# Performance work log

Measured on AMD Instinct MI355X. Metric: run time of the kernel, lower is better.

## Reference

```python
import jax, jax.numpy as jnp
import numpy as np
import math

D_MODEL = 1024
N_HEADS = 16
D_K = D_MODEL // N_HEADS
FFN = 4096
B, S = 4, 1024
EPS = 1e-5


def setup_inputs() -> dict:
    key = jax.random.key(0)
    ks = jax.random.split(key, 24)
    sd = 0.02
    def w(k, shape):
        return jax.random.normal(k, shape, dtype=jnp.float32) * sd
    inp = {
        'x': jax.random.normal(ks[0], (B, S, D_MODEL), dtype=jnp.float32),
        'enc': jax.random.normal(ks[1], (B, S, D_MODEL), dtype=jnp.float32),
        'mask': jnp.tril(jnp.ones((S, S), dtype=jnp.int32)),  # causal look-ahead mask
        # stacked per-head projections [H, d_model, d_k], biases [H, d_k]
        'Wq_self': w(ks[2], (N_HEADS, D_MODEL, D_K)), 'bq_self': w(ks[3], (N_HEADS, D_K)),
        'Wk_self': w(ks[4], (N_HEADS, D_MODEL, D_K)), 'bk_self': w(ks[5], (N_HEADS, D_K)),
        'Wv_self': w(ks[6], (N_HEADS, D_MODEL, D_K)), 'bv_self': w(ks[7], (N_HEADS, D_K)),
        'Wq_x': w(ks[8], (N_HEADS, D_MODEL, D_K)), 'bq_x': w(ks[9], (N_HEADS, D_K)),
        'Wk_x': w(ks[10], (N_HEADS, D_MODEL, D_K)), 'bk_x': w(ks[11], (N_HEADS, D_K)),
        'Wv_x': w(ks[12], (N_HEADS, D_MODEL, D_K)), 'bv_x': w(ks[13], (N_HEADS, D_K)),
        # W_O is SHARED between self- and cross-attention (as in the torch code)
        'Wo': w(ks[14], (D_MODEL, D_MODEL)), 'bo': w(ks[15], (D_MODEL,)),
        'W1': w(ks[16], (D_MODEL, FFN)), 'b1': w(ks[17], (FFN,)),
        'W2': w(ks[18], (FFN, D_MODEL)), 'b2': w(ks[19], (D_MODEL,)),
        'g1': jnp.ones((D_MODEL,), jnp.float32), 'be1': jnp.zeros((D_MODEL,), jnp.float32),
        'g2': jnp.ones((D_MODEL,), jnp.float32), 'be2': jnp.zeros((D_MODEL,), jnp.float32),
        'g3': jnp.ones((D_MODEL,), jnp.float32), 'be3': jnp.zeros((D_MODEL,), jnp.float32),
    }
    return inp


def _layernorm(x, g, b):
    mu = jnp.mean(x, axis=-1, keepdims=True)
    d = x - mu
    var = jnp.mean(d * d, axis=-1, keepdims=True)
    return d * jax.lax.rsqrt(var + EPS) * g + b


def _mha(xq, xkv, Wq, bq, Wk, bk, Wv, bv, mask):
    # batched equivalent of the per-head Python loop
    q = jnp.einsum('bsd,hdk->bhsk', xq, Wq) + bq[None, :, None, :]
    k = jnp.einsum('btd,hdk->bhtk', xkv, Wk) + bk[None, :, None, :]
    v = jnp.einsum('btd,hdk->bhtk', xkv, Wv) + bv[None, :, None, :]
    scores = jnp.einsum('bhsk,bhtk->bhst', q, k) / math.sqrt(D_K)
    if mask is not None:
        scores = jnp.where(mask[None, None] == 0, -jnp.inf, scores)
    attn = jax.nn.softmax(scores, axis=-1)
    z = jnp.einsum('bhst,bhtk->bhsk', attn, v)
    # concat heads along last dim (head i occupies slice i, matching torch.cat)
    b_, h_, s_, k_ = z.shape
    return jnp.transpose(z, (0, 2, 1, 3)).reshape(b_, s_, h_ * k_)


def reference(x, enc, mask, Wq_self, bq_self, Wk_self, bk_self, Wv_self, bv_self,
              Wq_x, bq_x, Wk_x, bk_x, Wv_x, bv_x, Wo, bo, W1, b1, W2, b2,
              g1, be1, g2, be2, g3, be3):
    sa = _mha(x, x, Wq_self, bq_self, Wk_self, bk_self, Wv_self, bv_self, mask)
    x1 = _layernorm(x + sa @ Wo + bo, g1, be1)
    ca = _mha(x1, enc, Wq_x, bq_x, Wk_x, bk_x, Wv_x, bv_x, None)
    x2 = _layernorm(x1 + ca @ Wo + bo, g2, be2)
    ffn = jax.nn.relu(x2 @ W1 + b1) @ W2 + b2
    return _layernorm(x2 + ffn, g3, be3)
```

## Files before the change

### kernel.cpp

```cpp
#include <hip/hip_runtime.h>
#include <cstdint>

typedef __bf16 bf16_t;
typedef bf16_t bf16x8 __attribute__((ext_vector_type(8)));
typedef bf16_t bf16x4 __attribute__((ext_vector_type(4)));
typedef float  f32x4  __attribute__((ext_vector_type(4)));

#define DEVI static __device__ __forceinline__

DEVI void async_ld16(const bf16_t* g, bf16_t* l) {
  __builtin_amdgcn_global_load_lds((const __attribute__((address_space(1))) void*)g,
                                   (__attribute__((address_space(3))) void*)l, 16, 0, 0);
}

struct PrepArgs {
  const float *WqS, *WkS, *WvS, *WqX, *WkX, *WvX, *Wo, *W1, *W2, *x, *enc;
  const float *bqS, *bkS, *bvS, *bkX, *bvX;
  bf16_t *WqkvST, *WqXT, *WkvXT, *WoT, *W1T, *W2T, *xb, *encb;
  float *bqkv, *bkvx;
};

__global__ __launch_bounds__(256)
void k_prep(PrepArgs a)
{
  __shared__ float tile[32][36];
  const int blk = blockIdx.x, tid = threadIdx.x;

  const float* src = nullptr;
  bf16_t* dst = nullptr;
  int srcLd = 0, dstLd = 0, m0 = 0, n0 = 0;
  bool do_tr = false;

  if (blk < 6144) {
    int j = blk >> 10, q = blk & 1023;
    src = j == 0 ? a.WqS : j == 1 ? a.WkS : j == 2 ? a.WvS : j == 3 ? a.WqX : j == 4 ? a.WkX : a.WvX;
    dst = j == 0 ? a.WqkvST : j == 1 ? a.WqkvST + 1048576 : j == 2 ? a.WqkvST + 2097152
        : j == 3 ? a.WqXT : j == 4 ? a.WkvXT : a.WkvXT + 1048576;
    int batch = q >> 6, rem = q & 63;
    src += (long)batch * 65536; dst += (long)batch * 65536;
    srcLd = 64; dstLd = 1024;
    n0 = (rem & 1) * 32; m0 = (rem >> 1) * 32;
    do_tr = true;
  } else if (blk < 7168) {
    int q = blk - 6144;
    src = a.Wo; dst = a.WoT; srcLd = 1024; dstLd = 1024;
    m0 = (q >> 5) * 32; n0 = (q & 31) * 32; do_tr = true;
  } else if (blk < 11264) {
    int q = blk - 7168;
    src = a.W1; dst = a.W1T; srcLd = 4096; dstLd = 1024;
    m0 = (q >> 7) * 32; n0 = (q & 127) * 32; do_tr = true;
  } else if (blk < 15360) {
    int q = blk - 11264;
    src = a.W2; dst = a.W2T; srcLd = 1024; dstLd = 4096;
    m0 = (q >> 5) * 32; n0 = (q & 31) * 32; do_tr = true;
  } else if (blk < 16384) {
    long base = (long)(blk - 15360) * 4096 + tid * 4;
#pragma unroll
    for (int u = 0; u < 4; u++) {
      float4 v = *(const float4*)(a.x + base + u * 1024);
      bf16x4 o; o[0] = (bf16_t)v.x; o[1] = (bf16_t)v.y; o[2] = (bf16_t)v.z; o[3] = (bf16_t)v.w;
      *(bf16x4*)(a.xb + base + u * 1024) = o;
    }
    return;
  } else if (blk < 17408) {
    long base = (long)(blk - 16384) * 4096 + tid * 4;
#pragma unroll
    for (int u = 0; u < 4; u++) {
      float4 v = *(const float4*)(a.enc + base + u * 1024);
      bf16x4 o; o[0] = (bf16_t)v.x; o[1] = (bf16_t)v.y; o[2] = (bf16_t)v.z; o[3] = (bf16_t)v.w;
      *(bf16x4*)(a.encb + base + u * 1024) = o;
    }
    return;
  } else {
    int gi = (blk - 17408) * 1024 + tid * 4;
#pragma unroll
    for (int j = 0; j < 4; j++) {
      int i = gi + j;
      if (i < 1024)      a.bqkv[i] = a.bqS[i];
      else if (i < 2048) a.bqkv[i] = a.bkS[i - 1024];
      else if (i < 3072) a.bqkv[i] = a.bvS[i - 2048];
      else if (i < 4096) a.bkvx[i - 3072] = a.bkX[i - 3072];
      else if (i < 5120) a.bkvx[i - 3072] = a.bvX[i - 4096];
    }
    return;
  }

  if (do_tr) {
    {
      int r = tid >> 3, c4 = (tid & 7) * 4;
      *(float4*)&tile[r][c4] = *(const float4*)(src + (long)(m0 + r) * srcLd + n0 + c4);
    }
    __syncthreads();
    {
      int nr = tid >> 3, mq = (tid & 7) * 4;
      bf16x4 o;
      o[0] = (bf16_t)tile[mq + 0][nr];
      o[1] = (bf16_t)tile[mq + 1][nr];
      o[2] = (bf16_t)tile[mq + 2][nr];
      o[3] = (bf16_t)tile[mq + 3][nr];
      *(bf16x4*)(dst + (long)(n0 + nr) * dstLd + m0 + mq) = o;
    }
  }
}

template<int OUT_MODE, int RELU, int VOFF>
__global__ __launch_bounds__(256, 2)
void k_gemm(const bf16_t* __restrict__ A, int lda,
            const bf16_t* __restrict__ Bt, int ldb,
            const float* __restrict__ bias,
            bf16_t* __restrict__ C, int ldc,
            bf16_t* __restrict__ Vt,
            bf16_t* __restrict__ p0, bf16_t* __restrict__ p1,
            bf16_t* __restrict__ p2, bf16_t* __restrict__ p3,
            int Ktot, int nx)
{
  __shared__ bf16_t As[2][128 * 32];
  __shared__ bf16_t Bs[2][128 * 32];
  const int tid  = threadIdx.x;
  const int wave = tid >> 6, lane = tid & 63;
  const int quad = lane >> 4, m16 = lane & 15;

  int lin = blockIdx.x;
  int perx = gridDim.x >> 3;
  int t = (lin & 7) * perx + (lin >> 3);
  const int bcol = (t % nx) * 128, brow = (t / nx) * 128;
  const int wr = (wave >> 1) * 64, wc = (wave & 1) * 64;

  const int Kper = Ktot / gridDim.z;
  const int k0 = blockIdx.z * Kper;

  f32x4 acc[4][4];
#pragma unroll
  for (int i = 0; i < 4; i++)
#pragma unroll
    for (int j = 0; j < 4; j++) acc[i][j] = (f32x4){0.f, 0.f, 0.f, 0.f};

  auto stage = [&](int kt, int buf) {
#pragma unroll
    for (int i = 0; i < 2; i++) {
      int rg = wave * 2 + i;
      async_ld16(A  + (long)(brow + rg * 16 + m16) * lda + kt + quad * 8, As[buf] + rg * 512);
      async_ld16(Bt + (long)(bcol + rg * 16 + m16) * ldb + kt + quad * 8, Bs[buf] + rg * 512);
    }
  };

  stage(k0, 0);
  __syncthreads();

  const int nIter = Kper >> 5;
  for (int it = 0; it < nIter; it++) {
    const int cur = it & 1;
    if (it + 1 < nIter) stage(k0 + (it + 1) * 32, cur ^ 1);

    bf16x8 af[4], bfr[4];
#pragma unroll
    for (int tt = 0; tt < 4; tt++) {
      af[tt]  = *(const bf16x8*)(As[cur] + ((wr + tt * 16) >> 4) * 512 + quad * 128 + m16 * 8);
      bfr[tt] = *(const bf16x8*)(Bs[cur] + ((wc + tt * 16) >> 4) * 512 + quad * 128 + m16 * 8);
    }
#pragma unroll
    for (int i = 0; i < 4; i++)
#pragma unroll
      for (int j = 0; j < 4; j++)
        acc[i][j] = __builtin_amdgcn_mfma_f32_16x16x32_bf16(af[i], bfr[j], acc[i][j], 0, 0, 0);

    __syncthreads();
  }

  if (OUT_MODE == 1) {
    bf16_t* P = blockIdx.z == 0 ? p0 : blockIdx.z == 1 ? p1 : blockIdx.z == 2 ? p2 : p3;
#pragma unroll
    for (int i = 0; i < 4; i++)
#pragma unroll
      for (int j = 0; j < 4; j++) {
        int col = bcol + wc + j * 16 + m16;
#pragma unroll
        for (int r = 0; r < 4; r++) {
          int row = brow + wr + i * 16 + quad * 4 + r;
          P[(long)row * ldc + col] = (bf16_t)acc[i][j][r];
        }
      }
  } else {
#pragma unroll
    for (int i = 0; i < 4; i++)
#pragma unroll
      for (int j = 0; j < 4; j++) {
        int col = bcol + wc + j * 16 + m16;
        float bv = bias[col];
        if (VOFF && col >= VOFF) {
          int hh = (col - VOFF) >> 6, dd = col & 63;
          int row0 = brow + wr + i * 16 + quad * 4;
          int bb = row0 >> 10, seq = row0 & 1023;
          bf16x4 pk;
#pragma unroll
          for (int r = 0; r < 4; r++) pk[r] = (bf16_t)(acc[i][j][r] + bv);
          *(bf16x4*)(Vt + (long)(bb * 16 + hh) * 65536 + dd * 1024 + seq) = pk;
        } else {
#pragma unroll
          for (int r = 0; r < 4; r++) {
            int row = brow + wr + i * 16 + quad * 4 + r;
            float v = acc[i][j][r] + bv;
            if (RELU) v = v > 0.f ? v : 0.f;
            C[(long)row * ldc + col] = (bf16_t)v;
          }
        }
      }
  }
}

template<int OUT_MODE, int RELU, int VOFF>
__global__ __launch_bounds__(512, 2)
void k_gemm256(const bf16_t* __restrict__ A, int lda,
               const bf16_t* __restrict__ Bt, int ldb,
               const float* __restrict__ bias,
               bf16_t* __restrict__ C, int ldc,
               bf16_t* __restrict__ Vt,
               bf16_t* __restrict__ p0, bf16_t* __restrict__ p1,
               bf16_t* __restrict__ p2, bf16_t* __restrict__ p3,
               int Ktot, int nx)
{
  __shared__ bf16_t As[2][256 * 64];
  __shared__ bf16_t Bs[2][256 * 64];
  const int tid  = threadIdx.x;
  const int wave = tid >> 6, lane = tid & 63;
  const int quad = lane >> 4, m16 = lane & 15;

  int lin = blockIdx.x;
  int perx = gridDim.x >> 3;
  int t = (lin & 7) * perx + (lin >> 3);
  const int bcol = (t % nx) * 256, brow = (t / nx) * 256;
  const int wr = (wave >> 2) * 128, wc = (wave & 3) * 64;

  const int Kper = Ktot / gridDim.z;
  const int k0 = blockIdx.z * Kper;

  f32x4 acc[8][4];
#pragma unroll
  for (int i = 0; i < 8; i++)
#pragma unroll
    for (int j = 0; j < 4; j++) acc[i][j] = (f32x4){0.f, 0.f, 0.f, 0.f};

  auto stage = [&](int kt, int buf) {
#pragma unroll
    for (int i = 0; i < 2; i++) {
      int rg = wave * 2 + i;
#pragma unroll
      for (int ks = 0; ks < 2; ks++) {
        async_ld16(A  + (long)(brow + rg * 16 + m16) * lda + kt + ks * 32 + quad * 8,
                   As[buf] + (rg * 2 + ks) * 512);
        async_ld16(Bt + (long)(bcol + rg * 16 + m16) * ldb + kt + ks * 32 + quad * 8,
                   Bs[buf] + (rg * 2 + ks) * 512);
      }
    }
  };

  stage(k0, 0);
  __syncthreads();

  const int nIter = Kper >> 6;
  for (int it = 0; it < nIter; it++) {
    const int cur = it & 1;
    if (it + 1 < nIter) stage(k0 + (it + 1) * 64, cur ^ 1);

    const bf16_t* Ac = As[cur];
    const bf16_t* Bc = Bs[cur];
#pragma unroll
    for (int ks = 0; ks < 2; ks++) {
      bf16x8 af[8], bfr[4];
#pragma unroll
      for (int tt = 0; tt < 8; tt++)
        af[tt] = *(const bf16x8*)(Ac + (((wr + tt * 16) >> 4) * 2 + ks) * 512 + quad * 128 + m16 * 8);
#pragma unroll
      for (int j = 0; j < 4; j++)
        bfr[j] = *(const bf16x8*)(Bc + (((wc + j * 16) >> 4) * 2 + ks) * 512 + quad * 128 + m16 * 8);
      __builtin_amdgcn_s_setprio(1);
#pragma unroll
      for (int i = 0; i < 8; i++)
#pragma unroll
        for (int j = 0; j < 4; j++)
          acc[i][j] = __builtin_amdgcn_mfma_f32_16x16x32_bf16(af[i], bfr[j], acc[i][j], 0, 0, 0);
      __builtin_amdgcn_s_setprio(0);
    }

    __syncthreads();
  }

  if (OUT_MODE == 1) {
    bf16_t* P = blockIdx.z == 0 ? p0 : blockIdx.z == 1 ? p1 : blockIdx.z == 2 ? p2 : p3;
#pragma unroll
    for (int i = 0; i < 8; i++)
#pragma unroll
      for (int j = 0; j < 4; j++) {
        int col = bcol + wc + j * 16 + m16;
#pragma unroll
        for (int r = 0; r < 4; r++) {
          int row = brow + wr + i * 16 + quad * 4 + r;
          P[(long)row * ldc + col] = (bf16_t)acc[i][j][r];
        }
      }
  } else {
#pragma unroll
    for (int i = 0; i < 8; i++)
#pragma unroll
      for (int j = 0; j < 4; j++) {
        int col = bcol + wc + j * 16 + m16;
        float bv = bias[col];
        if (VOFF && col >= VOFF) {
          int hh = (col - VOFF) >> 6, dd = col & 63;
          int row0 = brow + wr + i * 16 + quad * 4;
          int bb = row0 >> 10, seq = row0 & 1023;
          bf16x4 pk;
#pragma unroll
          for (int r = 0; r < 4; r++) pk[r] = (bf16_t)(acc[i][j][r] + bv);
          *(bf16x4*)(Vt + (long)(bb * 16 + hh) * 65536 + dd * 1024 + seq) = pk;
        } else {
#pragma unroll
          for (int r = 0; r < 4; r++) {
            int row = brow + wr + i * 16 + quad * 4 + r;
            float v = acc[i][j][r] + bv;
            if (RELU) v = v > 0.f ? v : 0.f;
            C[(long)row * ldc + col] = (bf16_t)v;
          }
        }
      }
  }
}

template<int LN, int RESID, int OUTF, int OUTB, int NPART>
__global__ __launch_bounds__(256)
void k_reduceN(const bf16_t* __restrict__ p0, const bf16_t* __restrict__ p1,
               const bf16_t* __restrict__ p2, const bf16_t* __restrict__ p3,
               const float* __restrict__ bias, const float* __restrict__ resid,
               const float* __restrict__ gamma, const float* __restrict__ beta,
               float* __restrict__ outf, bf16_t* __restrict__ outb)
{
  constexpr int D = 1024;
  __shared__ float red[8];
  int row = blockIdx.x, tid = threadIdx.x;
  long off = (long)row * D + tid * 4;
  bf16x4 a0 = *(const bf16x4*)(p0 + off);
  bf16x4 a1 = *(const bf16x4*)(p1 + off);
  float4 bb4 = *(const float4*)(bias + tid * 4);
  float4 v;
  v.x = (float)a0[0] + (float)a1[0] + bb4.x;
  v.y = (float)a0[1] + (float)a1[1] + bb4.y;
  v.z = (float)a0[2] + (float)a1[2] + bb4.z;
  v.w = (float)a0[3] + (float)a1[3] + bb4.w;
  if (NPART == 4) {
    bf16x4 a2 = *(const bf16x4*)(p2 + off);
    bf16x4 a3 = *(const bf16x4*)(p3 + off);
    v.x += (float)a2[0] + (float)a3[0];
    v.y += (float)a2[1] + (float)a3[1];
    v.z += (float)a2[2] + (float)a3[2];
    v.w += (float)a2[3] + (float)a3[3];
  }
  if (RESID) {
    float4 q = *(const float4*)(resid + off);
    v.x += q.x; v.y += q.y; v.z += q.z; v.w += q.w;
  }
  float4 y = v;
  if (LN) {
    float s  = v.x + v.y + v.z + v.w;
    float sq = v.x * v.x + v.y * v.y + v.z * v.z + v.w * v.w;
#pragma unroll
    for (int o = 1; o < 64; o <<= 1) {
      s  += __shfl_xor(s, o, 64);
      sq += __shfl_xor(sq, o, 64);
    }
    int wave = tid >> 6, lane = tid & 63;
    if (lane == 0) { red[wave * 2] = s; red[wave * 2 + 1] = sq; }
    __syncthreads();
    float ts = red[0] + red[2] + red[4] + red[6];
    float tq = red[1] + red[3] + red[5] + red[7];
    float mu = ts * (1.f / D);
    float var = tq * (1.f / D) - mu * mu;
    float rstd = rsqrtf(var + 1e-5f);
    float4 g  = *(const float4*)(gamma + tid * 4);
    float4 be = *(const float4*)(beta + tid * 4);
    y.x = (v.x - mu) * rstd * g.x + be.x;
    y.y = (v.y - mu) * rstd * g.y + be.y;
    y.z = (v.z - mu) * rstd * g.z + be.z;
    y.w = (v.w - mu) * rstd * g.w + be.w;
  }
  if (OUTF) *(float4*)(outf + off) = y;
  if (OUTB) {
    bf16x4 o;
    o[0] = (bf16_t)y.x; o[1] = (bf16_t)y.y; o[2] = (bf16_t)y.z; o[3] = (bf16_t)y.w;
    *(bf16x4*)(outb + off) = o;
  }
}

template<int CAUSAL>
__global__ __launch_bounds__(256, 2)
void k_attn(const bf16_t* __restrict__ Q, int ldq,
            const bf16_t* __restrict__ Kp, int ldk,
            const bf16_t* __restrict__ Vt,
            bf16_t* __restrict__ O)
{
  constexpr int S = 1024;
  __shared__ bf16_t Kls[2][4096];
  __shared__ bf16_t Vls[2][4096];
  __shared__ bf16_t Pls[4][32 * 72];

  const int tid = threadIdx.x;
  const int wave = tid >> 6, lane = tid & 63;
  const int quad = lane >> 4, m16 = lane & 15;
  const int bh = blockIdx.y, b = bh >> 4, h = bh & 15;
  const int qt = (CAUSAL && (bh & 32)) ? ((int)gridDim.x - 1 - (int)blockIdx.x)
                                       : (int)blockIdx.x;
  const int qbase = qt * 128 + wave * 32;

  bf16x8 qf[2][2];
#pragma unroll
  for (int rh = 0; rh < 2; rh++) {
    const bf16_t* qp = Q + (long)(b * S + qbase + rh * 16 + m16) * ldq + h * 64 + quad * 8;
    qf[rh][0] = *(const bf16x8*)qp;
    qf[rh][1] = *(const bf16x8*)(qp + 32);
  }

  f32x4 o_acc[2][4];
#pragma unroll
  for (int rh = 0; rh < 2; rh++)
#pragma unroll
    for (int t = 0; t < 4; t++) o_acc[rh][t] = (f32x4){0.f, 0.f, 0.f, 0.f};
  float rsum[2][4];
#pragma unroll
  for (int rh = 0; rh < 2; rh++)
#pragma unroll
    for (int r = 0; r < 4; r++) rsum[rh][r] = 0.f;

  auto stage = [&](int c, int buf) {
#pragma unroll
    for (int i = 0; i < 2; i++) {
      int t2 = wave * 2 + i;
      int rg = t2 & 3, ph = t2 >> 2;
      async_ld16(Kp + (long)(b * S + c * 64 + rg * 16 + m16) * ldk + h * 64 + ph * 32 + quad * 8,
                 Kls[buf] + t2 * 512);
      async_ld16(Vt + (long)bh * 65536 + (rg * 16 + m16) * 1024 + c * 64 + ph * 32 + quad * 8,
                 Vls[buf] + t2 * 512);
    }
  };

  const int nch = CAUSAL ? (2 * qt + 2) : 16;
  stage(0, 0);

  for (int c = 0; c < nch; c++) {
    __syncthreads();
    const int cur = c & 1;
    if (c + 1 < nch) stage(c + 1, cur ^ 1);

    f32x4 s[2][4];
#pragma unroll
    for (int t = 0; t < 4; t++) {
      bf16x8 k0 = *(const bf16x8*)(Kls[cur] + (0 * 4 + t) * 512 + quad * 128 + m16 * 8);
      bf16x8 k1 = *(const bf16x8*)(Kls[cur] + (1 * 4 + t) * 512 + quad * 128 + m16 * 8);
      __builtin_amdgcn_s_setprio(1);
#pragma unroll
      for (int rh = 0; rh < 2; rh++) {
        f32x4 z = (f32x4){0.f, 0.f, 0.f, 0.f};
        z = __builtin_amdgcn_mfma_f32_16x16x32_bf16(qf[rh][0], k0, z, 0, 0, 0);
        z = __builtin_amdgcn_mfma_f32_16x16x32_bf16(qf[rh][1], k1, z, 0, 0, 0);
        s[rh][t] = z;
      }
      __builtin_amdgcn_s_setprio(0);
    }

    bf16_t* pw = Pls[wave];
#pragma unroll
    for (int rh = 0; rh < 2; rh++)
#pragma unroll
      for (int r = 0; r < 4; r++) {
        int qg = qbase + rh * 16 + quad * 4 + r;
#pragma unroll
        for (int t = 0; t < 4; t++) {
          float v = s[rh][t][r] * 0.125f;
          float p;
          if (CAUSAL) {
            int kvg = c * 64 + t * 16 + m16;
            p = (kvg <= qg) ? __expf(v) : 0.f;
          } else {
            p = __expf(v);
          }
          rsum[rh][r] += p;
          pw[(rh * 16 + quad * 4 + r) * 72 + t * 16 + m16] = (bf16_t)p;
        }
      }

    bf16x8 pf[2][2];
#pragma unroll
    for (int rh = 0; rh < 2; rh++)
#pragma unroll
      for (int kvh = 0; kvh < 2; kvh++)
        pf[rh][kvh] = *(const bf16x8*)(pw + (rh * 16 + m16) * 72 + kvh * 32 + quad * 8);
#pragma unroll
    for (int t = 0; t < 4; t++) {
      bf16x8 v0 = *(const bf16x8*)(Vls[cur] + (0 * 4 + t) * 512 + quad * 128 + m16 * 8);
      bf16x8 v1 = *(const bf16x8*)(Vls[cur] + (1 * 4 + t) * 512 + quad * 128 + m16 * 8);
      __builtin_amdgcn_s_setprio(1);
#pragma unroll
      for (int rh = 0; rh < 2; rh++) {
        o_acc[rh][t] = __builtin_amdgcn_mfma_f32_16x16x32_bf16(pf[rh][0], v0, o_acc[rh][t], 0, 0, 0);
        o_acc[rh][t] = __builtin_amdgcn_mfma_f32_16x16x32_bf16(pf[rh][1], v1, o_acc[rh][t], 0, 0, 0);
      }
      __builtin_amdgcn_s_setprio(0);
    }
  }

#pragma unroll
  for (int rh = 0; rh < 2; rh++)
#pragma unroll
    for (int r = 0; r < 4; r++) {
      float v = rsum[rh][r];
      v += __shfl_xor(v, 1, 64);
      v += __shfl_xor(v, 2, 64);
      v += __shfl_xor(v, 4, 64);
      v += __shfl_xor(v, 8, 64);
      rsum[rh][r] = 1.f / v;
    }
#pragma unroll
  for (int rh = 0; rh < 2; rh++)
#pragma unroll
    for (int t = 0; t < 4; t++)
#pragma unroll
      for (int r = 0; r < 4; r++) {
        int row = b * S + qbase + rh * 16 + quad * 4 + r;
        int col = h * 64 + t * 16 + m16;
        O[(long)row * 1024 + col] = (bf16_t)(o_acc[rh][t][r] * rsum[rh][r]);
      }
}

extern "C" void kernel_launch(void* const* d_in, const int* in_sizes, int n_in,
                              void* d_out, int out_size, void* d_ws, size_t ws_size,
                              hipStream_t stream)
{
  const float* x   = (const float*)d_in[0];
  const float* enc = (const float*)d_in[1];
  const float* WqS = (const float*)d_in[3];
  const float* bqS = (const float*)d_in[4];
  const float* WkS = (const float*)d_in[5];
  const float* bkS = (const float*)d_in[6];
  const float* WvS = (const float*)d_in[7];
  const float* bvS = (const float*)d_in[8];
  const float* WqX = (const float*)d_in[9];
  const float* bqX = (const float*)d_in[10];
  const float* WkX = (const float*)d_in[11];
  const float* bkX = (const float*)d_in[12];
  const float* WvX = (const float*)d_in[13];
  const float* bvX = (const float*)d_in[14];
  const float* Wo  = (const float*)d_in[15];
  const float* bo  = (const float*)d_in[16];
  const float* W1  = (const float*)d_in[17];
  const float* b1  = (const float*)d_in[18];
  const float* W2  = (const float*)d_in[19];
  const float* b2  = (const float*)d_in[20];
  const float* g1  = (const float*)d_in[21];
  const float* be1 = (const float*)d_in[22];
  const float* g2  = (const float*)d_in[23];
  const float* be2 = (const float*)d_in[24];
  const float* g3  = (const float*)d_in[25];
  const float* be3 = (const float*)d_in[26];

  char* ws = (char*)d_ws;
  const long MBy = 1048576;
  bf16_t* WqkvST = (bf16_t*)(ws + 0 * MBy);
  bf16_t* WqXT   = (bf16_t*)(ws + 6 * MBy);
  bf16_t* WkvXT  = (bf16_t*)(ws + 8 * MBy);
  bf16_t* WoT    = (bf16_t*)(ws + 12 * MBy);
  bf16_t* W1T    = (bf16_t*)(ws + 14 * MBy);
  bf16_t* W2T    = (bf16_t*)(ws + 22 * MBy);
  float*  bqkvS  = (float*)(ws + 30 * MBy);
  float*  bkvX   = (float*)(ws + 30 * MBy + 16384);
  bf16_t* xb     = (bf16_t*)(ws + 31 * MBy);
  bf16_t* Qx     = xb;
  bf16_t* encb   = (bf16_t*)(ws + 39 * MBy);
  float*  x1f    = (float*)(ws + 47 * MBy);
  bf16_t* x1b    = (bf16_t*)(ws + 63 * MBy);
  bf16_t* Z      = (bf16_t*)(ws + 71 * MBy);
  bf16_t* QK     = (bf16_t*)(ws + 79 * MBy);
  bf16_t* Kenc   = (bf16_t*)(ws + 79 * MBy);
  bf16_t* Vt     = (bf16_t*)(ws + 95 * MBy);
  bf16_t* pa0 = (bf16_t*)(ws + 95 * MBy);
  bf16_t* pa1 = (bf16_t*)(ws + 103 * MBy);
  bf16_t* Hbuf = (bf16_t*)(ws + 95 * MBy);
  bf16_t* pf0 = (bf16_t*)(ws + 0 * MBy);
  bf16_t* pf1 = (bf16_t*)(ws + 8 * MBy);
  bf16_t* pf2 = (bf16_t*)(ws + 31 * MBy);
  bf16_t* pf3 = (bf16_t*)(ws + 39 * MBy);

  dim3 tb(256), tb512(512);

  PrepArgs pa;
  pa.WqS = WqS; pa.WkS = WkS; pa.WvS = WvS; pa.WqX = WqX; pa.WkX = WkX; pa.WvX = WvX;
  pa.Wo = Wo; pa.W1 = W1; pa.W2 = W2; pa.x = x; pa.enc = enc;
  pa.bqS = bqS; pa.bkS = bkS; pa.bvS = bvS; pa.bkX = bkX; pa.bvX = bvX;
  pa.WqkvST = WqkvST; pa.WqXT = WqXT; pa.WkvXT = WkvXT; pa.WoT = WoT;
  pa.W1T = W1T; pa.W2T = W2T; pa.xb = xb; pa.encb = encb;
  pa.bqkv = bqkvS; pa.bkvx = bkvX;
  k_prep<<<dim3(17413), tb, 0, stream>>>(pa);

  k_gemm<0, 0, 2048><<<dim3(768, 1, 1), tb, 0, stream>>>(
      xb, 1024, WqkvST, 1024, bqkvS, QK, 2048, Vt,
      nullptr, nullptr, nullptr, nullptr, 1024, 24);
  k_attn<1><<<dim3(8, 64), tb, 0, stream>>>(QK, 2048, QK + 1024, 2048, Vt, Z);
  k_gemm<1, 0, 0><<<dim3(256, 1, 2), tb, 0, stream>>>(
      Z, 1024, WoT, 1024, nullptr, nullptr, 1024, nullptr,
      pa0, pa1, nullptr, nullptr, 1024, 8);
  k_reduceN<1, 1, 1, 1, 2><<<dim3(4096), tb, 0, stream>>>(
      pa0, pa1, nullptr, nullptr, bo, x, g1, be1, x1f, x1b);

  k_gemm<1, 0, 0><<<dim3(256, 1, 2), tb, 0, stream>>>(
      x1b, 1024, WqXT, 1024, nullptr, nullptr, 1024, nullptr,
      pa0, pa1, nullptr, nullptr, 1024, 8);
  k_reduceN<0, 0, 0, 1, 2><<<dim3(4096), tb, 0, stream>>>(
      pa0, pa1, nullptr, nullptr, bqX, nullptr, nullptr, nullptr, nullptr, Qx);
  k_gemm<0, 0, 1024><<<dim3(512, 1, 1), tb, 0, stream>>>(
      encb, 1024, WkvXT, 1024, bkvX, Kenc, 1024, Vt,
      nullptr, nullptr, nullptr, nullptr, 1024, 16);
  k_attn<0><<<dim3(8, 64), tb, 0, stream>>>(Qx, 1024, Kenc, 1024, Vt, Z);
  k_gemm<1, 0, 0><<<dim3(256, 1, 2), tb, 0, stream>>>(
      Z, 1024, WoT, 1024, nullptr, nullptr, 1024, nullptr,
      pa0, pa1, nullptr, nullptr, 1024, 8);
  k_reduceN<1, 1, 1, 1, 2><<<dim3(4096), tb, 0, stream>>>(
      pa0, pa1, nullptr, nullptr, bo, x1f, g2, be2, x1f, x1b);

  k_gemm256<0, 1, 0><<<dim3(256, 1, 1), tb512, 0, stream>>>(
      x1b, 1024, W1T, 1024, b1, Hbuf, 4096, nullptr,
      nullptr, nullptr, nullptr, nullptr, 1024, 16);
  k_gemm256<1, 0, 0><<<dim3(64, 1, 4), tb512, 0, stream>>>(
      Hbuf, 4096, W2T, 4096, nullptr, nullptr, 1024, nullptr,
      pf0, pf1, pf2, pf3, 4096, 4);
  k_reduceN<1, 1, 1, 0, 4><<<dim3(4096), tb, 0, stream>>>(
      pf0, pf1, pf2, pf3, b2, x1f, g3, be3, (float*)d_out, nullptr);
}
```

Measured before the change: 546.1 us.

## Merge cross-attention Q and KV projections into one dual GEMM launch

Adds a dual-role GEMM kernel whose blocks split by index into the Qx projection (from x1) and the encoder K/V projection, so both run in one launch without the split-K partials and reduction pass for Qx. The self-attention QKV projection also moves to the larger 256-tile GEMM kernel with fewer blocks. This removes two launches and a round trip through partial buffers, and fills the GPU with the union of both grids. In exchange, the new kernel uses smaller 128x128 tiles with K-step 32 and no split-K, and the bigger tile for QKV leaves fewer blocks to spread across CUs.

After: 538.4 us. No clear change (-1.4%).

```diff
diff --git a/kernel.cpp b/kernel.cpp
--- a/kernel.cpp
+++ b/kernel.cpp
@@ -206,6 +206,97 @@
         }
       }
   }
+}
+
+__global__ __launch_bounds__(256, 2)
+void k_gemm_dual(const bf16_t* __restrict__ Aa, const bf16_t* __restrict__ Bta,
+                 const float* __restrict__ biasa, bf16_t* __restrict__ Ca,
+                 int nxa, int nblkA,
+                 const bf16_t* __restrict__ Ab, const bf16_t* __restrict__ Btb,
+                 const float* __restrict__ biasb, bf16_t* __restrict__ Cb,
+                 int nxb,
+                 bf16_t* __restrict__ Vt)
+{
+  __shared__ bf16_t As[2][128 * 32];
+  __shared__ bf16_t Bs[2][128 * 32];
+  const int tid  = threadIdx.x;
+  const int wave = tid >> 6, lane = tid & 63;
+  const int quad = lane >> 4, m16 = lane & 15;
+
+  const bool roleB = (int)blockIdx.x >= nblkA;
+  const bf16_t* A    = roleB ? Ab    : Aa;
+  const bf16_t* Bt   = roleB ? Btb   : Bta;
+  const float*  bias = roleB ? biasb : biasa;
+  bf16_t*       C    = roleB ? Cb    : Ca;
+  const int nx   = roleB ? nxb : nxa;
+  const int lin  = roleB ? ((int)blockIdx.x - nblkA) : (int)blockIdx.x;
+  const int nblk = roleB ? ((int)gridDim.x - nblkA) : nblkA;
+  const int perx = nblk >> 3;
+  const int t = (lin & 7) * perx + (lin >> 3);
+  const int bcol = (t % nx) * 128, brow = (t / nx) * 128;
+  const int wr = (wave >> 1) * 64, wc = (wave & 1) * 64;
+  const int lda = 1024, ldb = 1024, ldc = 1024;
+
+  f32x4 acc[4][4];
+#pragma unroll
+  for (int i = 0; i < 4; i++)
+#pragma unroll
+    for (int j = 0; j < 4; j++) acc[i][j] = (f32x4){0.f, 0.f, 0.f, 0.f};
+
+  auto stage = [&](int kt, int buf) {
+#pragma unroll
+    for (int i = 0; i < 2; i++) {
+      int rg = wave * 2 + i;
+      async_ld16(A  + (long)(brow + rg * 16 + m16) * lda + kt + quad * 8, As[buf] + rg * 512);
+      async_ld16(Bt + (long)(bcol + rg * 16 + m16) * ldb + kt + quad * 8, Bs[buf] + rg * 512);
+    }
+  };
+
+  stage(0, 0);
+  __syncthreads();
+
+  const int nIter = 32;
+  for (int it = 0; it < nIter; it++) {
+    const int cur = it & 1;
+    if (it + 1 < nIter) stage((it + 1) * 32, cur ^ 1);
+
+    bf16x8 af[4], bfr[4];
+#pragma unroll
+    for (int tt = 0; tt < 4; tt++) {
+      af[tt]  = *(const bf16x8*)(As[cur] + ((wr + tt * 16) >> 4) * 512 + quad * 128 + m16 * 8);
+      bfr[tt] = *(const bf16x8*)(Bs[cur] + ((wc + tt * 16) >> 4) * 512 + quad * 128 + m16 * 8);
+    }
+#pragma unroll
+    for (int i = 0; i < 4; i++)
+#pragma unroll
+      for (int j = 0; j < 4; j++)
+        acc[i][j] = __builtin_amdgcn_mfma_f32_16x16x32_bf16(af[i], bfr[j], acc[i][j], 0, 0, 0);
+
+    __syncthreads();
+  }
+
+#pragma unroll
+  for (int i = 0; i < 4; i++)
+#pragma unroll
+    for (int j = 0; j < 4; j++) {
+      int col = bcol + wc + j * 16 + m16;
+      float bv = bias[col];
+      if (col >= 1024) {
+        int hh = (col - 1024) >> 6, dd = col & 63;
+        int row0 = brow + wr + i * 16 + quad * 4;
+        int bb = row0 >> 10, seq = row0 & 1023;
+        bf16x4 pk;
+#pragma unroll
+        for (int r = 0; r < 4; r++) pk[r] = (bf16_t)(acc[i][j][r] + bv);
+        *(bf16x4*)(Vt + (long)(bb * 16 + hh) * 65536 + dd * 1024 + seq) = pk;
+      } else {
+#pragma unroll
+        for (int r = 0; r < 4; r++) {
+          int row = brow + wr + i * 16 + quad * 4 + r;
+          C[(long)row * ldc + col] = (bf16_t)(acc[i][j][r] + bv);
+        }
+      }
+    }
 }
 
 template<int OUT_MODE, int RELU, int VOFF>
@@ -598,9 +689,9 @@
   pa.bqkv = bqkvS; pa.bkvx = bkvX;
   k_prep<<<dim3(17413), tb, 0, stream>>>(pa);
 
-  k_gemm<0, 0, 2048><<<dim3(768, 1, 1), tb, 0, stream>>>(
+  k_gemm256<0, 0, 2048><<<dim3(192, 1, 1), tb512, 0, stream>>>(
       xb, 1024, WqkvST, 1024, bqkvS, QK, 2048, Vt,
-      nullptr, nullptr, nullptr, nullptr, 1024, 24);
+      nullptr, nullptr, nullptr, nullptr, 1024, 12);
   k_attn<1><<<dim3(8, 64), tb, 0, stream>>>(QK, 2048, QK + 1024, 2048, Vt, Z);
   k_gemm<1, 0, 0><<<dim3(256, 1, 2), tb, 0, stream>>>(
       Z, 1024, WoT, 1024, nullptr, nullptr, 1024, nullptr,
@@ -608,14 +699,9 @@
   k_reduceN<1, 1, 1, 1, 2><<<dim3(4096), tb, 0, stream>>>(
       pa0, pa1, nullptr, nullptr, bo, x, g1, be1, x1f, x1b);
 
-  k_gemm<1, 0, 0><<<dim3(256, 1, 2), tb, 0, stream>>>(
-      x1b, 1024, WqXT, 1024, nullptr, nullptr, 1024, nullptr,
-      pa0, pa1, nullptr, nullptr, 1024, 8);
-  k_reduceN<0, 0, 0, 1, 2><<<dim3(4096), tb, 0, stream>>>(
-      pa0, pa1, nullptr, nullptr, bqX, nullptr, nullptr, nullptr, nullptr, Qx);
-  k_gemm<0, 0, 1024><<<dim3(512, 1, 1), tb, 0, stream>>>(
-      encb, 1024, WkvXT, 1024, bkvX, Kenc, 1024, Vt,
-      nullptr, nullptr, nullptr, nullptr, 1024, 16);
+  k_gemm_dual<<<dim3(768), tb, 0, stream>>>(
+      x1b, WqXT, bqX, Qx, 8, 256,
+      encb, WkvXT, bkvX, Kenc, 16, Vt);
   k_attn<0><<<dim3(8, 64), tb, 0, stream>>>(Qx, 1024, Kenc, 1024, Vt, Z);
   k_gemm<1, 0, 0><<<dim3(256, 1, 2), tb, 0, stream>>>(
       Z, 1024, WoT, 1024, nullptr, nullptr, 1024, nullptr,
```
